# Kernel optimization log

Hardware: AMD Instinct MI355X
Metric: run time of the kernel (lower is better)

Reference implementation:

```python
import jax, jax.numpy as jnp
import numpy as np

USER = 1000
CATE = 1400
FEAT = 128
B = 8192


def setup_inputs() -> dict:
    key = jax.random.key(0)
    ks = jax.random.split(key, 16)
    s = 0.05
    return {
        "feat": jax.random.normal(ks[0], (B, FEAT), jnp.float32),
        "fcat": jax.random.randint(ks[1], (B, 3), 0, CATE),
        "fusr": jax.random.randint(ks[2], (B,), 0, USER),
        "fitm": jax.random.randint(ks[3], (B,), 0, USER),
        "flg": 1,
        "usr_w": jax.random.normal(ks[4], (USER, 128), jnp.float32) * s,
        "cate_w": jax.random.normal(ks[5], (CATE, 11), jnp.float32) * s,
        "cmat_w": jax.random.normal(ks[6], (CATE, 11 * 11), jnp.float32) * s,
        "cbias_w": jax.random.normal(ks[7], (CATE, 11), jnp.float32) * s,
        "ubias_w": jax.random.normal(ks[8], (USER, 128), jnp.float32) * s,
        "cbiasb_w": jax.random.normal(ks[9], (CATE, 95), jnp.float32) * s,
        "fc0_w": jax.random.normal(ks[10], (95, FEAT), jnp.float32) * s,
        "fc0_b": jax.random.normal(ks[11], (95,), jnp.float32) * s,
        "cvismat_w": jax.random.normal(ks[12], (CATE, 95 * 95), jnp.float32) * s,
        "cvisbias_w": jax.random.normal(ks[13], (CATE, 95), jnp.float32) * s,
    }


def reference(feat, fcat, fusr, fitm, flg, usr_w, cate_w, cmat_w, cbias_w,
              ubias_w, cbiasb_w, fc0_w, fc0_b, cvismat_w, cvisbias_w):
    b = feat.shape[0]
    c0, c1, c2 = fcat[:, 0], fcat[:, 1], fcat[:, 2]
    # cat1.repeat(1,11)*cmat .view(b,11,11).sum(2) == batched matvec M @ v
    cat1 = cate_w[c0]                                              # [b,11]
    cat2 = jnp.einsum('bij,bj->bi', cmat_w[c1].reshape(b, 11, 11), cat1) + cbias_w[c1]
    cat3 = jnp.einsum('bij,bj->bi', cmat_w[c2].reshape(b, 11, 11), cat2) + cbias_w[c2]
    cbias = jnp.concatenate([jnp.zeros((b, 33), feat.dtype), cbiasb_w[c2]], axis=1)  # [b,128]
    p0 = feat @ fc0_w.T + fc0_b                                    # [b,95]
    itmq = jnp.einsum('bij,bj->bi', cvismat_w[c2].reshape(b, 95, 95), p0) + cvisbias_w[c2]
    pitm = jnp.concatenate([cat1, cat2, cat3, itmq], axis=1)       # [b,128]
    if flg == 0:
        return jnp.sum((pitm + ubias_w[fusr]) * (usr_w[fusr] + cbias), axis=1).reshape(-1, 1)
    # flg != 0: score against all USER users; algebraic expansion avoids [b,USER,128]
    # sum_d (pitm[b,d]+ubias[u,d])*(usr[u,d]+cbias[b,d])
    return (pitm @ usr_w.T
            + jnp.sum(pitm * cbias, axis=1, keepdims=True)
            + jnp.sum(ubias_w * usr_w, axis=1)[None, :]
            + cbias @ ubias_w.T)                                    # [b,USER]
```

## Files before the change

### kernel.cpp

```cpp
#include <hip/hip_runtime.h>
#include <hip/hip_bf16.h>

typedef unsigned short u16;
typedef unsigned int u32;
typedef u16 u16x4 __attribute__((ext_vector_type(4)));
typedef u16 u16x8 __attribute__((ext_vector_type(8)));
typedef __bf16 bf16x8 __attribute__((ext_vector_type(8)));
typedef float f32x4 __attribute__((ext_vector_type(4)));

#define USER_N 1000
#define CATE_N 1400
#define FEAT_N 128
#define B_N 8192
#define CAP 64

__device__ __forceinline__ float b2f(u16 u) {
    union { u32 i; float f; } v; v.i = ((u32)u) << 16; return v.f;
}
__device__ __forceinline__ u16 f2b(float f) {
    union { float f; u32 i; } v; v.f = f;
    u32 x = v.i;
    u32 r = (x + 0x7fffu + ((x >> 16) & 1u)) >> 16;
    return (u16)r;
}
__device__ __forceinline__ f32x4 ld4u(const float* p) {
    f32x4 v; __builtin_memcpy(&v, p, 16); return v;
}
__device__ __forceinline__ bf16x8 cvt8(f32x4 a, f32x4 b) {
    u16x8 r = {f2b(a.x), f2b(a.y), f2b(a.z), f2b(a.w),
               f2b(b.x), f2b(b.y), f2b(b.z), f2b(b.w)};
    return __builtin_bit_cast(bf16x8, r);
}
__device__ __forceinline__ size_t xa_addr(int b, int k) {
    return (size_t)(b >> 4) * 4096 + (size_t)(k >> 3) * 128 + (b & 15) * 8 + (k & 7);
}

__global__ __launch_bounds__(256) void pack_kernel(
    const float* __restrict__ usr_w, const float* __restrict__ ubias_w,
    u16* __restrict__ WB, float* __restrict__ t, int* __restrict__ counts)
{
    if (blockIdx.x == 0) {
        for (int i = threadIdx.x; i < CATE_N; i += 256) counts[i] = 0;
    }
    const int gid = blockIdx.x * 256 + threadIdx.x;
    const int u = gid >> 5;
    const int l = gid & 31;
    if (u >= 1024) return;
    float part = 0.f;
    u16x4 wa = {0, 0, 0, 0}, wb = {0, 0, 0, 0};
    if (u < USER_N) {
        f32x4 a4 = *(const f32x4*)&usr_w[u * 128 + l * 4];
        f32x4 b4 = *(const f32x4*)&ubias_w[u * 128 + l * 4];
        wa = (u16x4){f2b(a4.x), f2b(a4.y), f2b(a4.z), f2b(a4.w)};
        wb = (u16x4){f2b(b4.x), f2b(b4.y), f2b(b4.z), f2b(b4.w)};
        part = a4.x * b4.x + a4.y * b4.y + a4.z * b4.z + a4.w * b4.w;
    }
    const int nb = u >> 4, lm = u & 15;
    const int ks = l >> 3, quad = (l >> 1) & 3, j0 = (l & 1) * 4;
    *(u16x4*)&WB[(size_t)(nb * 8 + ks) * 512 + quad * 128 + lm * 8 + j0] = wa;
    *(u16x4*)&WB[(size_t)(nb * 8 + 4 + ks) * 512 + quad * 128 + lm * 8 + j0] = wb;
    part += __shfl_xor(part, 16, 32);
    part += __shfl_xor(part, 8, 32);
    part += __shfl_xor(part, 4, 32);
    part += __shfl_xor(part, 2, 32);
    part += __shfl_xor(part, 1, 32);
    if (l == 0) t[u] = part;
}

__global__ __launch_bounds__(256) void bin_kernel(
    const int* __restrict__ fcat, int* __restrict__ counts,
    int* __restrict__ bins)
{
    const int gid = blockIdx.x * 256 + threadIdx.x;
    if (gid < B_N) {
        int c2 = fcat[gid * 3 + 2];
        int slot = atomicAdd(&counts[c2], 1);
        if (slot < CAP) bins[c2 * CAP + slot] = gid;
    }
}

__global__ __launch_bounds__(128) void p0chain_kernel(
    const float* __restrict__ feat, const int* __restrict__ fcat,
    const float* __restrict__ cate_w, const float* __restrict__ cmat_w,
    const float* __restrict__ cbias_w, const float* __restrict__ fc0_w,
    const float* __restrict__ fc0_b,
    float* __restrict__ p0G, u16* __restrict__ XA)
{
    const int tid = threadIdx.x;
    const int wave = tid >> 6, lane = tid & 63;
    const int lm = lane & 15, quad = lane >> 4;
    const int mt = blockIdx.x * 2 + wave;
    const int b0 = mt * 16;

    bf16x8 a[4];
    const float* frw = feat + (size_t)(b0 + lm) * 128 + quad * 8;
    #pragma unroll
    for (int ks = 0; ks < 4; ++ks)
        a[ks] = cvt8(*(const f32x4*)(frw + ks * 32),
                     *(const f32x4*)(frw + ks * 32 + 4));

    #pragma unroll
    for (int nt = 0; nt < 6; ++nt) {
        const int i = nt * 16 + lm;
        const bool v = (i < 95);
        const float* br = fc0_w + (size_t)(v ? i : 0) * 128 + quad * 8;
        f32x4 acc = {0.f, 0.f, 0.f, 0.f};
        #pragma unroll
        for (int ks = 0; ks < 4; ++ks) {
            f32x4 lo = {0,0,0,0}, hi = {0,0,0,0};
            if (v) { lo = *(const f32x4*)(br + ks * 32);
                     hi = *(const f32x4*)(br + ks * 32 + 4); }
            acc = __builtin_amdgcn_mfma_f32_16x16x32_bf16(a[ks], cvt8(lo, hi),
                                                          acc, 0, 0, 0);
        }
        const float bias = v ? fc0_b[i] : 0.f;
        #pragma unroll
        for (int r = 0; r < 4; ++r) {
            int row = b0 + quad * 4 + r;
            p0G[(size_t)row * 96 + i] = v ? (acc[r] + bias) : 0.f;
        }
    }

    __shared__ float chainS[2][16][36];
    const int r = lm;
    const int bq = b0 + r;
    const int c0 = fcat[bq * 3 + 0], c1 = fcat[bq * 3 + 1], c2 = fcat[bq * 3 + 2];

    #pragma unroll
    for (int dd = 0; dd < 3; ++dd) {
        int d = quad + dd * 4;
        if (d < 11) chainS[wave][r][d] = cate_w[c0 * 11 + d];
    }
    __syncthreads();
    float st[3];
    #pragma unroll
    for (int dd = 0; dd < 3; ++dd) {
        int d = quad + dd * 4;
        if (d < 11) {
            float acc = cbias_w[c1 * 11 + d];
            #pragma unroll
            for (int j = 0; j < 11; ++j)
                acc += cmat_w[c1 * 121 + d * 11 + j] * chainS[wave][r][j];
            st[dd] = acc;
        }
    }
    #pragma unroll
    for (int dd = 0; dd < 3; ++dd) {
        int d = quad + dd * 4;
        if (d < 11) chainS[wave][r][11 + d] = st[dd];
    }
    __syncthreads();
    #pragma unroll
    for (int dd = 0; dd < 3; ++dd) {
        int d = quad + dd * 4;
        if (d < 11) {
            float acc = cbias_w[c2 * 11 + d];
            #pragma unroll
            for (int j = 0; j < 11; ++j)
                acc += cmat_w[c2 * 121 + d * 11 + j] * chainS[wave][r][11 + j];
            st[dd] = acc;
        }
    }
    #pragma unroll
    for (int dd = 0; dd < 3; ++dd) {
        int d = quad + dd * 4;
        if (d < 11) chainS[wave][r][22 + d] = st[dd];
    }
    __syncthreads();
    for (int idx = lane; idx < 16 * 33; idx += 64) {
        int r2 = idx / 33, cc = idx - r2 * 33;
        int bb = b0 + r2;
        XA[xa_addr(bb, cc)] = f2b(chainS[wave][r2][cc]);
        XA[xa_addr(bb, 128 + cc)] = 0;
    }
}

__global__ __launch_bounds__(128) void itmq_kernel(
    const float* __restrict__ cvismat_w, const float* __restrict__ cvisbias_w,
    const float* __restrict__ cbiasb_w,
    const int* __restrict__ counts, const int* __restrict__ bins,
    const float* __restrict__ p0G,
    u16* __restrict__ XA, float* __restrict__ s_out)
{
    const int c = blockIdx.x;
    int n = counts[c];
    if (n <= 0) return;
    if (n > CAP) n = CAP;
    const int tid = threadIdx.x;
    const int wave = tid >> 6, lane = tid & 63;
    const int lm = lane & 15, quad = lane >> 4;

    __shared__ float qS[16 * 96];
    __shared__ float cvbS[96], cbbS[96];
    __shared__ u16   cbb16S[96];
    __shared__ int   brS[16];

    if (tid < 96) cvbS[tid] = (tid < 95) ? cvisbias_w[c * 95 + tid] : 0.f;
    if (tid >= 32) {
        int k = tid - 32;
        float v = (k < 95) ? cbiasb_w[c * 95 + k] : 0.f;
        cbbS[k] = v;
        cbb16S[k] = f2b(v);
    }

    bf16x8 bfr[3][3];
    #pragma unroll
    for (int tnt = 0; tnt < 3; ++tnt) {
        const int i = (wave * 3 + tnt) * 16 + lm;
        const bool v = (i < 95);
        const float* br = cvismat_w + (size_t)c * 9025 + (size_t)(v ? i : 0) * 95;
        #pragma unroll
        for (int ks = 0; ks < 3; ++ks) {
            f32x4 lo = {0,0,0,0}, hi = {0,0,0,0};
            if (v) {
                if (ks < 2 || quad < 3) {
                    lo = ld4u(br + ks * 32 + quad * 8);
                    hi = ld4u(br + ks * 32 + quad * 8 + 4);
                } else {
                    lo = ld4u(br + 88);
                    hi.x = br[92]; hi.y = br[93]; hi.z = br[94]; hi.w = 0.f;
                }
            }
            bfr[tnt][ks] = cvt8(lo, hi);
        }
    }

    for (int m0 = 0; m0 < n; m0 += 16) {
        const int am = m0 + lm;
        const int ab = bins[c * CAP + (am < n ? am : 0)];
        const float* pr = p0G + (size_t)ab * 96 + quad * 8;
        bf16x8 a[3];
        #pragma unroll
        for (int ks = 0; ks < 3; ++ks)
            a[ks] = cvt8(*(const f32x4*)(pr + ks * 32),
                         *(const f32x4*)(pr + ks * 32 + 4));
        f32x4 acc[3] = {{0,0,0,0}, {0,0,0,0}, {0,0,0,0}};
        #pragma unroll
        for (int tnt = 0; tnt < 3; ++tnt)
            #pragma unroll
            for (int ks = 0; ks < 3; ++ks)
                acc[tnt] = __builtin_amdgcn_mfma_f32_16x16x32_bf16(
                    a[ks], bfr[tnt][ks], acc[tnt], 0, 0, 0);

        __syncthreads();
        if (tid < 16) brS[tid] = bins[c * CAP + ((m0 + tid < n) ? m0 + tid : 0)];
        #pragma unroll
        for (int tnt = 0; tnt < 3; ++tnt) {
            const int i = (wave * 3 + tnt) * 16 + lm;
            #pragma unroll
            for (int r = 0; r < 4; ++r)
                qS[(quad * 4 + r) * 96 + i] = acc[tnt][r] + cvbS[i];
        }
        __syncthreads();

        {
            const int rr = tid >> 3, q8 = tid & 7;
            float p = 0.f;
            if (m0 + rr < n)
                for (int i = q8; i < 95; i += 8) p += qS[rr * 96 + i] * cbbS[i];
            p += __shfl_xor(p, 4, 8);
            p += __shfl_xor(p, 2, 8);
            p += __shfl_xor(p, 1, 8);
            if (q8 == 0 && m0 + rr < n) s_out[brS[rr]] = p;
        }
        const int nv = min(16, n - m0);
        for (int idx = tid; idx < nv * 95; idx += 128) {
            int r2 = idx / 95;
            int col = idx - r2 * 95;
            int bb = brS[r2];
            XA[xa_addr(bb, 33 + col)] = f2b(qS[r2 * 96 + col]);
            XA[xa_addr(bb, 161 + col)] = cbb16S[col];
        }
    }
}

__global__ __launch_bounds__(256) void gemm_kernel(
    const u16* __restrict__ XA, const u16* __restrict__ WB,
    const float* __restrict__ s, const float* __restrict__ t,
    float* __restrict__ out)
{
    const int tid = threadIdx.x;
    const int wave = tid >> 6;
    const int lane = tid & 63;
    const int lm = lane & 15;
    const int quad = lane >> 4;
    const int lofs = quad * 128 + lm * 8;

    const int mb = blockIdx.x * 4 + wave;
    const u16* abase = XA + (size_t)mb * 4096;
    const u16* wb0 = WB + (size_t)(blockIdx.y * 4 + 0) * 4096;
    const u16* wb1 = WB + (size_t)(blockIdx.y * 4 + 1) * 4096;
    const u16* wb2 = WB + (size_t)(blockIdx.y * 4 + 2) * 4096;
    const u16* wb3 = WB + (size_t)(blockIdx.y * 4 + 3) * 4096;

    f32x4 acc0 = {0.f, 0.f, 0.f, 0.f};
    f32x4 acc1 = {0.f, 0.f, 0.f, 0.f};
    f32x4 acc2 = {0.f, 0.f, 0.f, 0.f};
    f32x4 acc3 = {0.f, 0.f, 0.f, 0.f};

    #pragma unroll 2
    for (int ks = 0; ks < 8; ++ks) {
        const int o = ks * 512 + lofs;
        bf16x8 a = __builtin_bit_cast(bf16x8, *(const u16x8*)(abase + o));
        bf16x8 b0 = __builtin_bit_cast(bf16x8, *(const u16x8*)(wb0 + o));
        bf16x8 b1 = __builtin_bit_cast(bf16x8, *(const u16x8*)(wb1 + o));
        bf16x8 b2 = __builtin_bit_cast(bf16x8, *(const u16x8*)(wb2 + o));
        bf16x8 b3 = __builtin_bit_cast(bf16x8, *(const u16x8*)(wb3 + o));
        acc0 = __builtin_amdgcn_mfma_f32_16x16x32_bf16(a, b0, acc0, 0, 0, 0);
        acc1 = __builtin_amdgcn_mfma_f32_16x16x32_bf16(a, b1, acc1, 0, 0, 0);
        acc2 = __builtin_amdgcn_mfma_f32_16x16x32_bf16(a, b2, acc2, 0, 0, 0);
        acc3 = __builtin_amdgcn_mfma_f32_16x16x32_bf16(a, b3, acc3, 0, 0, 0);
    }

    const int m0 = mb * 16;
    float sv[4];
    #pragma unroll
    for (int r = 0; r < 4; ++r) sv[r] = s[m0 + quad * 4 + r];

    f32x4 accs[4] = {acc0, acc1, acc2, acc3};
    #pragma unroll
    for (int nf = 0; nf < 4; ++nf) {
        int u = blockIdx.y * 64 + nf * 16 + lm;
        if (u < USER_N) {
            float tv = t[u];
            #pragma unroll
            for (int r = 0; r < 4; ++r) {
                int ob = m0 + quad * 4 + r;
                out[(size_t)ob * USER_N + u] = accs[nf][r] + sv[r] + tv;
            }
        }
    }
}

extern "C" void kernel_launch(void* const* d_in, const int* in_sizes, int n_in,
                              void* d_out, int out_size, void* d_ws, size_t ws_size,
                              hipStream_t stream) {
    const float* feat      = (const float*)d_in[0];
    const int*   fcat      = (const int*)d_in[1];
    const float* usr_w     = (const float*)d_in[5];
    const float* cate_w    = (const float*)d_in[6];
    const float* cmat_w    = (const float*)d_in[7];
    const float* cbias_w   = (const float*)d_in[8];
    const float* ubias_w   = (const float*)d_in[9];
    const float* cbiasb_w  = (const float*)d_in[10];
    const float* fc0_w     = (const float*)d_in[11];
    const float* fc0_b     = (const float*)d_in[12];
    const float* cvismat_w = (const float*)d_in[13];
    const float* cvisbias_w= (const float*)d_in[14];
    float* out = (float*)d_out;

    char* ws = (char*)d_ws;
    u16*   XA     = (u16*)(ws);
    u16*   WB     = (u16*)(ws + 4194304);
    float* s      = (float*)(ws + 4718592);
    float* t      = (float*)(ws + 4751360);
    int*   counts = (int*)(ws + 4755456);
    int*   bins   = (int*)(ws + 4761056);
    float* p0G    = (float*)(ws + 5119456);

    pack_kernel<<<128, 256, 0, stream>>>(usr_w, ubias_w, WB, t, counts);
    bin_kernel<<<32, 256, 0, stream>>>(fcat, counts, bins);
    p0chain_kernel<<<256, 128, 0, stream>>>(feat, fcat, cate_w, cmat_w,
                                            cbias_w, fc0_w, fc0_b, p0G, XA);
    itmq_kernel<<<CATE_N, 128, 0, stream>>>(cvismat_w, cvisbias_w, cbiasb_w,
                                            counts, bins, p0G, XA, s);
    gemm_kernel<<<dim3(128, 16), 256, 0, stream>>>(XA, WB, s, t, out);
}
```

Measured before the change: 160.7 us.

## Prepack feat and fc0 to bf16, fuse binning into p0chain, widen GEMM tiles

Several changes at once. feat and fc0_w are converted to bf16 MFMA-fragment layouts inside the pack kernel, and the separate bin kernel is merged into p0chain, dropping one launch. p0 is stored as bf16 instead of fp32, halving its write and read traffic in itmq, and the chain step now uses per-wave waitcnt fences instead of block barriers. The final GEMM has each wave compute 8 user tiles instead of 4, which raises A reuse and register use; the atomic binning now depends on pack having zeroed counts one launch earlier.

```diff
diff --git a/kernel.cpp b/kernel.cpp
--- a/kernel.cpp
+++ b/kernel.cpp
@@ -37,140 +37,179 @@
 
 __global__ __launch_bounds__(256) void pack_kernel(
     const float* __restrict__ usr_w, const float* __restrict__ ubias_w,
-    u16* __restrict__ WB, float* __restrict__ t, int* __restrict__ counts)
+    const float* __restrict__ feat, const float* __restrict__ fc0_w,
+    u16* __restrict__ WB, float* __restrict__ t, int* __restrict__ counts,
+    u16* __restrict__ FA, u16* __restrict__ WF)
 {
-    if (blockIdx.x == 0) {
-        for (int i = threadIdx.x; i < CATE_N; i += 256) counts[i] = 0;
-    }
-    const int gid = blockIdx.x * 256 + threadIdx.x;
-    const int u = gid >> 5;
-    const int l = gid & 31;
-    if (u >= 1024) return;
-    float part = 0.f;
-    u16x4 wa = {0, 0, 0, 0}, wb = {0, 0, 0, 0};
-    if (u < USER_N) {
-        f32x4 a4 = *(const f32x4*)&usr_w[u * 128 + l * 4];
-        f32x4 b4 = *(const f32x4*)&ubias_w[u * 128 + l * 4];
-        wa = (u16x4){f2b(a4.x), f2b(a4.y), f2b(a4.z), f2b(a4.w)};
-        wb = (u16x4){f2b(b4.x), f2b(b4.y), f2b(b4.z), f2b(b4.w)};
-        part = a4.x * b4.x + a4.y * b4.y + a4.z * b4.z + a4.w * b4.w;
-    }
-    const int nb = u >> 4, lm = u & 15;
-    const int ks = l >> 3, quad = (l >> 1) & 3, j0 = (l & 1) * 4;
-    *(u16x4*)&WB[(size_t)(nb * 8 + ks) * 512 + quad * 128 + lm * 8 + j0] = wa;
-    *(u16x4*)&WB[(size_t)(nb * 8 + 4 + ks) * 512 + quad * 128 + lm * 8 + j0] = wb;
-    part += __shfl_xor(part, 16, 32);
-    part += __shfl_xor(part, 8, 32);
-    part += __shfl_xor(part, 4, 32);
-    part += __shfl_xor(part, 2, 32);
-    part += __shfl_xor(part, 1, 32);
-    if (l == 0) t[u] = part;
-}
-
-__global__ __launch_bounds__(256) void bin_kernel(
-    const int* __restrict__ fcat, int* __restrict__ counts,
-    int* __restrict__ bins)
-{
-    const int gid = blockIdx.x * 256 + threadIdx.x;
-    if (gid < B_N) {
-        int c2 = fcat[gid * 3 + 2];
-        int slot = atomicAdd(&counts[c2], 1);
-        if (slot < CAP) bins[c2 * CAP + slot] = gid;
-    }
-}
-
-__global__ __launch_bounds__(128) void p0chain_kernel(
-    const float* __restrict__ feat, const int* __restrict__ fcat,
+    const int bx = blockIdx.x;
+    const int tid = threadIdx.x;
+    if (bx < 128) {
+        if (bx == 0) {
+            for (int i = tid; i < CATE_N; i += 256) counts[i] = 0;
+        }
+        const int gid = bx * 256 + tid;
+        const int u = gid >> 5;
+        const int l = gid & 31;
+        float part = 0.f;
+        u16x4 wa = {0, 0, 0, 0}, wb = {0, 0, 0, 0};
+        if (u < USER_N) {
+            f32x4 a4 = *(const f32x4*)&usr_w[u * 128 + l * 4];
+            f32x4 b4 = *(const f32x4*)&ubias_w[u * 128 + l * 4];
+            wa = (u16x4){f2b(a4.x), f2b(a4.y), f2b(a4.z), f2b(a4.w)};
+            wb = (u16x4){f2b(b4.x), f2b(b4.y), f2b(b4.z), f2b(b4.w)};
+            part = a4.x * b4.x + a4.y * b4.y + a4.z * b4.z + a4.w * b4.w;
+        }
+        const int nb = u >> 4, lm = u & 15;
+        const int ks = l >> 3, quad = (l >> 1) & 3, j0 = (l & 1) * 4;
+        *(u16x4*)&WB[(size_t)(nb * 8 + ks) * 512 + quad * 128 + lm * 8 + j0] = wa;
+        *(u16x4*)&WB[(size_t)(nb * 8 + 4 + ks) * 512 + quad * 128 + lm * 8 + j0] = wb;
+        part += __shfl_xor(part, 16, 32);
+        part += __shfl_xor(part, 8, 32);
+        part += __shfl_xor(part, 4, 32);
+        part += __shfl_xor(part, 2, 32);
+        part += __shfl_xor(part, 1, 32);
+        if (l == 0) t[u] = part;
+    } else if (bx < 256) {
+        const int lm = tid >> 4;
+        const int q4 = tid & 15;
+        const int ks = q4 >> 2, quad = q4 & 3;
+        #pragma unroll
+        for (int it = 0; it < 4; ++it) {
+            const int mt = (bx - 128) * 4 + it;
+            const float* fr = feat + (size_t)(mt * 16 + lm) * 128 + ks * 32 + quad * 8;
+            f32x4 lo = *(const f32x4*)fr;
+            f32x4 hi = *(const f32x4*)(fr + 4);
+            *(u16x8*)&FA[(size_t)mt * 2048 + ks * 512 + quad * 128 + lm * 8] =
+                __builtin_bit_cast(u16x8, cvt8(lo, hi));
+        }
+    } else {
+        const int lm = tid & 15;
+        const int quad = (tid >> 4) & 3;
+        const int ks = tid >> 6;
+        #pragma unroll
+        for (int nt = 0; nt < 6; ++nt) {
+            const int i = nt * 16 + lm;
+            const bool v = (i < 95);
+            f32x4 lo = {0, 0, 0, 0}, hi = {0, 0, 0, 0};
+            if (v) {
+                const float* br = fc0_w + (size_t)i * 128 + ks * 32 + quad * 8;
+                lo = *(const f32x4*)br;
+                hi = *(const f32x4*)(br + 4);
+            }
+            *(u16x8*)&WF[(size_t)(nt * 4 + ks) * 512 + quad * 128 + lm * 8] =
+                __builtin_bit_cast(u16x8, cvt8(lo, hi));
+        }
+    }
+}
+
+__global__ __launch_bounds__(256) void p0chain_kernel(
+    const int* __restrict__ fcat,
     const float* __restrict__ cate_w, const float* __restrict__ cmat_w,
-    const float* __restrict__ cbias_w, const float* __restrict__ fc0_w,
-    const float* __restrict__ fc0_b,
-    float* __restrict__ p0G, u16* __restrict__ XA)
+    const float* __restrict__ cbias_w, const float* __restrict__ fc0_b,
+    const u16* __restrict__ FA, const u16* __restrict__ WF,
+    int* __restrict__ counts, int* __restrict__ bins,
+    u16* __restrict__ p0Gb, u16* __restrict__ XA)
 {
     const int tid = threadIdx.x;
-    const int wave = tid >> 6, lane = tid & 63;
+    const int w = tid >> 6, lane = tid & 63;
     const int lm = lane & 15, quad = lane >> 4;
-    const int mt = blockIdx.x * 2 + wave;
-    const int b0 = mt * 16;
-
+    const int b0 = blockIdx.x * 32;
+
+    if (tid < 32) {
+        int row = b0 + tid;
+        int c2v = fcat[row * 3 + 2];
+        int slot = atomicAdd(&counts[c2v], 1);
+        if (slot < CAP) bins[c2v * CAP + slot] = row;
+    }
+
+    const int mt = blockIdx.x * 2 + (w >> 1);
+    const int nth = w & 1;
     bf16x8 a[4];
-    const float* frw = feat + (size_t)(b0 + lm) * 128 + quad * 8;
+    const u16* fa = FA + (size_t)mt * 2048 + quad * 128 + lm * 8;
     #pragma unroll
     for (int ks = 0; ks < 4; ++ks)
-        a[ks] = cvt8(*(const f32x4*)(frw + ks * 32),
-                     *(const f32x4*)(frw + ks * 32 + 4));
-
-    #pragma unroll
-    for (int nt = 0; nt < 6; ++nt) {
+        a[ks] = __builtin_bit_cast(bf16x8, *(const u16x8*)(fa + ks * 512));
+
+    #pragma unroll
+    for (int nt3 = 0; nt3 < 3; ++nt3) {
+        const int nt = nth * 3 + nt3;
+        const u16* wf = WF + (size_t)(nt * 4) * 512 + quad * 128 + lm * 8;
+        f32x4 acc = {0.f, 0.f, 0.f, 0.f};
+        #pragma unroll
+        for (int ks = 0; ks < 4; ++ks)
+            acc = __builtin_amdgcn_mfma_f32_16x16x32_bf16(
+                a[ks], __builtin_bit_cast(bf16x8, *(const u16x8*)(wf + ks * 512)),
+                acc, 0, 0, 0);
         const int i = nt * 16 + lm;
         const bool v = (i < 95);
-        const float* br = fc0_w + (size_t)(v ? i : 0) * 128 + quad * 8;
-        f32x4 acc = {0.f, 0.f, 0.f, 0.f};
-        #pragma unroll
-        for (int ks = 0; ks < 4; ++ks) {
-            f32x4 lo = {0,0,0,0}, hi = {0,0,0,0};
-            if (v) { lo = *(const f32x4*)(br + ks * 32);
-                     hi = *(const f32x4*)(br + ks * 32 + 4); }
-            acc = __builtin_amdgcn_mfma_f32_16x16x32_bf16(a[ks], cvt8(lo, hi),
-                                                          acc, 0, 0, 0);
-        }
         const float bias = v ? fc0_b[i] : 0.f;
         #pragma unroll
         for (int r = 0; r < 4; ++r) {
-            int row = b0 + quad * 4 + r;
-            p0G[(size_t)row * 96 + i] = v ? (acc[r] + bias) : 0.f;
-        }
-    }
-
-    __shared__ float chainS[2][16][36];
-    const int r = lm;
-    const int bq = b0 + r;
-    const int c0 = fcat[bq * 3 + 0], c1 = fcat[bq * 3 + 1], c2 = fcat[bq * 3 + 2];
-
-    #pragma unroll
-    for (int dd = 0; dd < 3; ++dd) {
-        int d = quad + dd * 4;
-        if (d < 11) chainS[wave][r][d] = cate_w[c0 * 11 + d];
-    }
-    __syncthreads();
-    float st[3];
-    #pragma unroll
-    for (int dd = 0; dd < 3; ++dd) {
-        int d = quad + dd * 4;
+            int row = mt * 16 + quad * 4 + r;
+            p0Gb[(size_t)row * 96 + i] = v ? f2b(acc[r] + bias) : (u16)0;
+        }
+    }
+
+    __shared__ float chS[4][8][34];
+    const int r8 = lane & 7, oct = lane >> 3;
+    const int row = b0 + w * 8 + r8;
+    const int c0 = fcat[row * 3 + 0];
+    const int c1 = fcat[row * 3 + 1];
+    const int c2 = fcat[row * 3 + 2];
+
+    #pragma unroll
+    for (int dd = 0; dd < 2; ++dd) {
+        int d = oct + dd * 8;
+        if (d < 11) chS[w][r8][d] = cate_w[c0 * 11 + d];
+    }
+    asm volatile("s_waitcnt lgkmcnt(0)" ::: "memory");
+    __builtin_amdgcn_sched_barrier(0);
+
+    float st[2];
+    #pragma unroll
+    for (int dd = 0; dd < 2; ++dd) {
+        int d = oct + dd * 8;
+        st[dd] = 0.f;
         if (d < 11) {
             float acc = cbias_w[c1 * 11 + d];
+            const float* cm = cmat_w + (size_t)c1 * 121 + d * 11;
             #pragma unroll
-            for (int j = 0; j < 11; ++j)
-                acc += cmat_w[c1 * 121 + d * 11 + j] * chainS[wave][r][j];
+            for (int j = 0; j < 11; ++j) acc += cm[j] * chS[w][r8][j];
             st[dd] = acc;
         }
     }
     #pragma unroll
-    for (int dd = 0; dd < 3; ++dd) {
-        int d = quad + dd * 4;
-        if (d < 11) chainS[wave][r][11 + d] = st[dd];
-    }
-    __syncthreads();
-    #pragma unroll
-    for (int dd = 0; dd < 3; ++dd) {
-        int d = quad + dd * 4;
+    for (int dd = 0; dd < 2; ++dd) {
+        int d = oct + dd * 8;
+        if (d < 11) chS[w][r8][11 + d] = st[dd];
+    }
+    asm volatile("s_waitcnt lgkmcnt(0)" ::: "memory");
+    __builtin_amdgcn_sched_barrier(0);
+
+    #pragma unroll
+    for (int dd = 0; dd < 2; ++dd) {
+        int d = oct + dd * 8;
+        st[dd] = 0.f;
         if (d < 11) {
             float acc = cbias_w[c2 * 11 + d];
+            const float* cm = cmat_w + (size_t)c2 * 121 + d * 11;
             #pragma unroll
-            for (int j = 0; j < 11; ++j)
-                acc += cmat_w[c2 * 121 + d * 11 + j] * chainS[wave][r][11 + j];
+            for (int j = 0; j < 11; ++j) acc += cm[j] * chS[w][r8][11 + j];
             st[dd] = acc;
         }
     }
     #pragma unroll
-    for (int dd = 0; dd < 3; ++dd) {
-        int d = quad + dd * 4;
-        if (d < 11) chainS[wave][r][22 + d] = st[dd];
-    }
-    __syncthreads();
-    for (int idx = lane; idx < 16 * 33; idx += 64) {
+    for (int dd = 0; dd < 2; ++dd) {
+        int d = oct + dd * 8;
+        if (d < 11) chS[w][r8][22 + d] = st[dd];
+    }
+    asm volatile("s_waitcnt lgkmcnt(0)" ::: "memory");
+    __builtin_amdgcn_sched_barrier(0);
+
+    for (int idx = lane; idx < 8 * 33; idx += 64) {
         int r2 = idx / 33, cc = idx - r2 * 33;
-        int bb = b0 + r2;
-        XA[xa_addr(bb, cc)] = f2b(chainS[wave][r2][cc]);
+        int bb = b0 + w * 8 + r2;
+        XA[xa_addr(bb, cc)] = f2b(chS[w][r2][cc]);
         XA[xa_addr(bb, 128 + cc)] = 0;
     }
 }
@@ -179,7 +218,7 @@
     const float* __restrict__ cvismat_w, const float* __restrict__ cvisbias_w,
     const float* __restrict__ cbiasb_w,
     const int* __restrict__ counts, const int* __restrict__ bins,
-    const float* __restrict__ p0G,
+    const u16* __restrict__ p0Gb,
     u16* __restrict__ XA, float* __restrict__ s_out)
 {
     const int c = blockIdx.x;
@@ -228,12 +267,11 @@
     for (int m0 = 0; m0 < n; m0 += 16) {
         const int am = m0 + lm;
         const int ab = bins[c * CAP + (am < n ? am : 0)];
-        const float* pr = p0G + (size_t)ab * 96 + quad * 8;
+        const u16* pr = p0Gb + (size_t)ab * 96 + quad * 8;
         bf16x8 a[3];
         #pragma unroll
         for (int ks = 0; ks < 3; ++ks)
-            a[ks] = cvt8(*(const f32x4*)(pr + ks * 32),
-                         *(const f32x4*)(pr + ks * 32 + 4));
+            a[ks] = __builtin_bit_cast(bf16x8, *(const u16x8*)(pr + ks * 32));
         f32x4 acc[3] = {{0,0,0,0}, {0,0,0,0}, {0,0,0,0}};
         #pragma unroll
         for (int tnt = 0; tnt < 3; ++tnt)
@@ -286,30 +324,27 @@
     const int quad = lane >> 4;
     const int lofs = quad * 128 + lm * 8;
 
-    const int mb = blockIdx.x * 4 + wave;
-    const u16* abase = XA + (size_t)mb * 4096;
-    const u16* wb0 = WB + (size_t)(blockIdx.y * 4 + 0) * 4096;
-    const u16* wb1 = WB + (size_t)(blockIdx.y * 4 + 1) * 4096;
-    const u16* wb2 = WB + (size_t)(blockIdx.y * 4 + 2) * 4096;
-    const u16* wb3 = WB + (size_t)(blockIdx.y * 4 + 3) * 4096;
-
-    f32x4 acc0 = {0.f, 0.f, 0.f, 0.f};
-    f32x4 acc1 = {0.f, 0.f, 0.f, 0.f};
-    f32x4 acc2 = {0.f, 0.f, 0.f, 0.f};
-    f32x4 acc3 = {0.f, 0.f, 0.f, 0.f};
+    const int bid = blockIdx.x;
+    const int g = bid & 7;
+    const int p = bid >> 3;
+    const int mb = p * 4 + wave;
+    const u16* abase = XA + (size_t)mb * 4096 + lofs;
+    const u16* bbase = WB + (size_t)(g * 8) * 4096 + lofs;
+
+    f32x4 acc[8];
+    #pragma unroll
+    for (int j = 0; j < 8; ++j) acc[j] = (f32x4){0.f, 0.f, 0.f, 0.f};
 
     #pragma unroll 2
     for (int ks = 0; ks < 8; ++ks) {
-        const int o = ks * 512 + lofs;
+        const int o = ks * 512;
         bf16x8 a = __builtin_bit_cast(bf16x8, *(const u16x8*)(abase + o));
-        bf16x8 b0 = __builtin_bit_cast(bf16x8, *(const u16x8*)(wb0 + o));
-        bf16x8 b1 = __builtin_bit_cast(bf16x8, *(const u16x8*)(wb1 + o));
-        bf16x8 b2 = __builtin_bit_cast(bf16x8, *(const u16x8*)(wb2 + o));
-        bf16x8 b3 = __builtin_bit_cast(bf16x8, *(const u16x8*)(wb3 + o));
-        acc0 = __builtin_amdgcn_mfma_f32_16x16x32_bf16(a, b0, acc0, 0, 0, 0);
-        acc1 = __builtin_amdgcn_mfma_f32_16x16x32_bf16(a, b1, acc1, 0, 0, 0);
-        acc2 = __builtin_amdgcn_mfma_f32_16x16x32_bf16(a, b2, acc2, 0, 0, 0);
-        acc3 = __builtin_amdgcn_mfma_f32_16x16x32_bf16(a, b3, acc3, 0, 0, 0);
+        #pragma unroll
+        for (int j = 0; j < 8; ++j) {
+            bf16x8 b = __builtin_bit_cast(bf16x8,
+                *(const u16x8*)(bbase + (size_t)j * 4096 + o));
+            acc[j] = __builtin_amdgcn_mfma_f32_16x16x32_bf16(a, b, acc[j], 0, 0, 0);
+        }
     }
 
     const int m0 = mb * 16;
@@ -317,16 +352,15 @@
     #pragma unroll
     for (int r = 0; r < 4; ++r) sv[r] = s[m0 + quad * 4 + r];
 
-    f32x4 accs[4] = {acc0, acc1, acc2, acc3};
-    #pragma unroll
-    for (int nf = 0; nf < 4; ++nf) {
-        int u = blockIdx.y * 64 + nf * 16 + lm;
+    #pragma unroll
+    for (int j = 0; j < 8; ++j) {
+        int u = g * 128 + j * 16 + lm;
         if (u < USER_N) {
             float tv = t[u];
             #pragma unroll
             for (int r = 0; r < 4; ++r) {
                 int ob = m0 + quad * 4 + r;
-                out[(size_t)ob * USER_N + u] = accs[nf][r] + sv[r] + tv;
+                out[(size_t)ob * USER_N + u] = acc[j][r] + sv[r] + tv;
             }
         }
     }
@@ -356,13 +390,16 @@
     float* t      = (float*)(ws + 4751360);
     int*   counts = (int*)(ws + 4755456);
     int*   bins   = (int*)(ws + 4761056);
-    float* p0G    = (float*)(ws + 5119456);
-
-    pack_kernel<<<128, 256, 0, stream>>>(usr_w, ubias_w, WB, t, counts);
-    bin_kernel<<<32, 256, 0, stream>>>(fcat, counts, bins);
-    p0chain_kernel<<<256, 128, 0, stream>>>(feat, fcat, cate_w, cmat_w,
-                                            cbias_w, fc0_w, fc0_b, p0G, XA);
+    u16*   p0Gb   = (u16*)(ws + 5119456);
+    u16*   FA     = (u16*)(ws + 6692320);
+    u16*   WF     = (u16*)(ws + 8789472);
+
+    pack_kernel<<<257, 256, 0, stream>>>(usr_w, ubias_w, feat, fc0_w,
+                                         WB, t, counts, FA, WF);
+    p0chain_kernel<<<256, 256, 0, stream>>>(fcat, cate_w, cmat_w, cbias_w,
+                                            fc0_b, FA, WF, counts, bins,
+                                            p0Gb, XA);
     itmq_kernel<<<CATE_N, 128, 0, stream>>>(cvismat_w, cvisbias_w, cbiasb_w,
-                                            counts, bins, p0G, XA, s);
-    gemm_kernel<<<dim3(128, 16), 256, 0, stream>>>(XA, WB, s, t, out);
-}
+                                            counts, bins, p0Gb, XA, s);
+    gemm_kernel<<<1024, 256, 0, stream>>>(XA, WB, s, t, out);
+}
```

After: 161.4 us. About the same (+0.5%).
